# Optimization experiments

Hardware: AMD Instinct MI355X
Metric: run time of the kernel (lower is better)

The kernel has to match this reference:

```python
import jax, jax.numpy as jnp
import numpy as np

EPS = 1e-07


def setup_inputs() -> dict:
    key = jax.random.key(0)
    k1, k2, k3, k4, k5, k6 = jax.random.split(key, 6)
    B, S, E = 128, 512, 64  # batch, seq_len == n_items, emb_size
    user_emb = jax.random.normal(k1, (B, S, E), dtype=jnp.float32)
    item_emb = jax.random.normal(k2, (B, S, E), dtype=jnp.float32)
    cluster_weights = jax.random.uniform(k3, (B, S, 1), dtype=jnp.float32)
    # binary keep-mask over sequence positions (multiplicative)
    last_item_mask = (jax.random.uniform(k4, (B, 1, S)) > 0.5).astype(jnp.float32)
    proj_w = jax.random.normal(k5, (1, 1), dtype=jnp.float32)
    proj_b = jax.random.normal(k6, (1,), dtype=jnp.float32)
    return {
        "user_emb": user_emb,
        "item_emb": item_emb,
        "cluster_weights": cluster_weights,
        "last_item_mask": last_item_mask,
        "proj_w": proj_w,
        "proj_b": proj_b,
    }


def reference(user_emb, item_emb, cluster_weights, last_item_mask, proj_w, proj_b):
    # L2-normalize with clamped norm (matches torch.clamp(norm, 1e-7))
    u = user_emb / jnp.maximum(jnp.linalg.norm(user_emb, axis=-1, keepdims=True), EPS)
    v = item_emb / jnp.maximum(jnp.linalg.norm(item_emb, axis=-1, keepdims=True), EPS)
    # cosine sim: [B, n_items, seq_len] (n_items == seq_len == S)
    cos = jnp.einsum("bse,bne->bns", u, v)
    # cluster_weights [B,S,1] broadcasts over the seq_len axis, indexed by dim1
    # (faithful to torch broadcast of [B,N,S,1] * [B,S,1,1] with N == S)
    sims = cos * cluster_weights  # [B,N,S]
    # Linear(1,1) + sigmoid applied elementwise (scalar affine)
    sims = jax.nn.sigmoid(sims * proj_w[0, 0] + proj_b[0])
    # permute to [B, seq_len, n_items], mask [B,1,S] broadcasts over last axis
    sims = jnp.swapaxes(sims, 1, 2) * last_item_mask
    # max over dim 2 -> [B, seq_len]
    return jnp.max(sims, axis=2)
```

## Files before the change

kernel.cpp:

```cpp
#include <hip/hip_runtime.h>
#include <hip/hip_bf16.h>
#include <math.h>

#define B_ 128
#define S_ 512
#define E_ 64
#define PAD_ 72

typedef short bf16x8 __attribute__((ext_vector_type(8)));
typedef float f32x4 __attribute__((ext_vector_type(4)));

__device__ __forceinline__ unsigned short f2b(float f) {
  __hip_bfloat16 h = __float2bfloat16(f);
  unsigned short u;
  __builtin_memcpy(&u, &h, 2);
  return u;
}

__device__ __forceinline__ void norm16_coalesced(
    const float* __restrict__ src,
    const float* __restrict__ scl,
    float w0, int c, int g, int lane,
    unsigned short* __restrict__ lds_base) {
  f32x4 x[4];
  float sn[4];
#pragma unroll
  for (int i = 0; i < 4; ++i) x[i] = *(const f32x4*)(src + i * 256 + lane * 4);
#pragma unroll
  for (int i = 0; i < 4; ++i)
    sn[i] = scl ? scl[i * 4 + g] * w0 : 1.0f;
#pragma unroll
  for (int i = 0; i < 4; ++i) {
    float ss = x[i][0] * x[i][0] + x[i][1] * x[i][1] +
               x[i][2] * x[i][2] + x[i][3] * x[i][3];
    ss += __shfl_xor(ss, 1); ss += __shfl_xor(ss, 2);
    ss += __shfl_xor(ss, 4); ss += __shfl_xor(ss, 8);
    float s = sn[i] / fmaxf(sqrtf(ss), 1e-7f);
    ushort4 o;
    o.x = f2b(x[i][0] * s); o.y = f2b(x[i][1] * s);
    o.z = f2b(x[i][2] * s); o.w = f2b(x[i][3] * s);
    *(ushort4*)(lds_base + (size_t)(i * 4 + g) * PAD_ + c * 4) = o;
  }
}

__global__ __launch_bounds__(1024) void fused_kernel(
    const float* __restrict__ ue, const float* __restrict__ ve,
    const float* __restrict__ cw, const float* __restrict__ mask,
    const float* __restrict__ pw, const float* __restrict__ pb,
    float* __restrict__ out) {
  __shared__ unsigned short vlds[S_ * PAD_];
  __shared__ unsigned short ulds[256 * PAD_];
  __shared__ float comb[4][256];

  const int bx = blockIdx.x;
  const int b = (bx & 7) * 16 + (bx >> 4);
  const int shalf = (bx >> 3) & 1;

  const int tid = threadIdx.x;
  const int wv = tid >> 6;
  const int lane = tid & 63;
  const int c = lane & 15;
  const int g = lane >> 4;
  const int ws = wv >> 2;
  const int wn = wv & 3;

  const float w0 = pw[0];
  const float* __restrict__ vb = ve + (size_t)b * S_ * E_;
  const float* __restrict__ cwb = cw + (size_t)b * S_;
  const float* __restrict__ ub = ue + ((size_t)b * S_ + shalf * 256) * E_;
  const float* __restrict__ mb = mask + (size_t)b * S_;

  const int vown = shalf * 256 + wv * 16;
  const int voth = (1 - shalf) * 256 + wv * 16;
  const int urow = wv * 16;

  float pen[8];
#pragma unroll
  for (int j = 0; j < 4; ++j) {
    pen[j] = (mb[(shalf * 16 + wn * 4 + j) * 16 + c] > 0.5f) ? 0.0f : -1e30f;
    pen[4 + j] =
        (mb[((1 - shalf) * 16 + wn * 4 + j) * 16 + c] > 0.5f) ? 0.0f : -1e30f;
  }

  norm16_coalesced(vb + (size_t)vown * E_, cwb + vown, w0, c, g, lane,
                   vlds + (size_t)vown * PAD_);
  norm16_coalesced(ub + (size_t)urow * E_, nullptr, 1.0f, c, g, lane,
                   ulds + (size_t)urow * PAD_);

  __syncthreads();

  const float* psrc = vb + (size_t)voth * E_;
  f32x4 y[4];
#pragma unroll
  for (int i = 0; i < 4; ++i) y[i] = *(const f32x4*)(psrc + i * 256 + lane * 4);
  float cwo[4];
#pragma unroll
  for (int i = 0; i < 4; ++i) cwo[i] = cwb[voth + i * 4 + g];

  const unsigned short* urp = ulds + (size_t)(ws * 64 + c) * PAD_ + g * 8;
  bf16x8 a[4][2];
#pragma unroll
  for (int st = 0; st < 4; ++st) {
    a[st][0] = *(const bf16x8*)(urp + st * 16 * PAD_);
    a[st][1] = *(const bf16x8*)(urp + st * 16 * PAD_ + 32);
  }

  float r[4][4];
#pragma unroll
  for (int st = 0; st < 4; ++st)
#pragma unroll
    for (int i = 0; i < 4; ++i) r[st][i] = -INFINITY;

#pragma unroll
  for (int j = 0; j < 4; ++j) {
    const int it = shalf * 16 + wn * 4 + j;
    const unsigned short* vr = vlds + (size_t)(it * 16 + c) * PAD_ + g * 8;
    bf16x8 b0 = *(const bf16x8*)(vr);
    bf16x8 b1 = *(const bf16x8*)(vr + 32);
    f32x4 ci = {pen[j], pen[j], pen[j], pen[j]};
#pragma unroll
    for (int st = 0; st < 4; ++st) {
      f32x4 acc = __builtin_amdgcn_mfma_f32_16x16x32_bf16(a[st][0], b0, ci, 0, 0, 0);
      acc = __builtin_amdgcn_mfma_f32_16x16x32_bf16(a[st][1], b1, acc, 0, 0, 0);
      r[st][0] = fmaxf(r[st][0], acc[0]);
      r[st][1] = fmaxf(r[st][1], acc[1]);
      r[st][2] = fmaxf(r[st][2], acc[2]);
      r[st][3] = fmaxf(r[st][3], acc[3]);
    }
  }

#pragma unroll
  for (int i = 0; i < 4; ++i) {
    float ss = y[i][0] * y[i][0] + y[i][1] * y[i][1] +
               y[i][2] * y[i][2] + y[i][3] * y[i][3];
    ss += __shfl_xor(ss, 1); ss += __shfl_xor(ss, 2);
    ss += __shfl_xor(ss, 4); ss += __shfl_xor(ss, 8);
    float s = (w0 * cwo[i]) / fmaxf(sqrtf(ss), 1e-7f);
    ushort4 o;
    o.x = f2b(y[i][0] * s); o.y = f2b(y[i][1] * s);
    o.z = f2b(y[i][2] * s); o.w = f2b(y[i][3] * s);
    *(ushort4*)(vlds + (size_t)(voth + i * 4 + g) * PAD_ + c * 4) = o;
  }

  __syncthreads();

#pragma unroll
  for (int j = 0; j < 4; ++j) {
    const int it = (1 - shalf) * 16 + wn * 4 + j;
    const unsigned short* vr = vlds + (size_t)(it * 16 + c) * PAD_ + g * 8;
    bf16x8 b0 = *(const bf16x8*)(vr);
    bf16x8 b1 = *(const bf16x8*)(vr + 32);
    f32x4 ci = {pen[4 + j], pen[4 + j], pen[4 + j], pen[4 + j]};
#pragma unroll
    for (int st = 0; st < 4; ++st) {
      f32x4 acc = __builtin_amdgcn_mfma_f32_16x16x32_bf16(a[st][0], b0, ci, 0, 0, 0);
      acc = __builtin_amdgcn_mfma_f32_16x16x32_bf16(a[st][1], b1, acc, 0, 0, 0);
      r[st][0] = fmaxf(r[st][0], acc[0]);
      r[st][1] = fmaxf(r[st][1], acc[1]);
      r[st][2] = fmaxf(r[st][2], acc[2]);
      r[st][3] = fmaxf(r[st][3], acc[3]);
    }
  }

#pragma unroll
  for (int st = 0; st < 4; ++st)
#pragma unroll
    for (int i = 0; i < 4; ++i) {
      float v = r[st][i];
      v = fmaxf(v, __shfl_xor(v, 1)); v = fmaxf(v, __shfl_xor(v, 2));
      v = fmaxf(v, __shfl_xor(v, 4)); v = fmaxf(v, __shfl_xor(v, 8));
      r[st][i] = v;
    }

  if (c == 0) {
#pragma unroll
    for (int st = 0; st < 4; ++st)
#pragma unroll
      for (int i = 0; i < 4; ++i)
        comb[wn][ws * 64 + st * 16 + g * 4 + i] = r[st][i];
  }

  __syncthreads();

  if (tid < 256) {
    float v = fmaxf(fmaxf(comb[0][tid], comb[1][tid]),
                    fmaxf(comb[2][tid], comb[3][tid]));
    float bias = pb[0];
    out[(size_t)b * S_ + shalf * 256 + tid] =
        (v < -1e29f) ? 0.0f : 1.0f / (1.0f + expf(-(v + bias)));
  }
}

extern "C" void kernel_launch(void* const* d_in, const int* in_sizes, int n_in,
                              void* d_out, int out_size, void* d_ws, size_t ws_size,
                              hipStream_t stream) {
  const float* ue = (const float*)d_in[0];
  const float* ve = (const float*)d_in[1];
  const float* cw = (const float*)d_in[2];
  const float* mask = (const float*)d_in[3];
  const float* pw = (const float*)d_in[4];
  const float* pb = (const float*)d_in[5];
  float* out = (float*)d_out;

  hipLaunchKernelGGL(fused_kernel, dim3(2 * B_), dim3(1024), 0, stream,
                     ue, ve, cw, mask, pw, pb, out);
}
```

Baseline: 17.53 us.

## Load user rows straight into MFMA fragments and defer normalization past max

User embeddings are no longer normalized into a shared-memory tile. Each lane loads its raw rows straight into bf16 MFMA A-fragments and computes the row inverse-norm with cross-lane shuffles. Because the per-row scale is positive, it is applied after the max reduction instead of before the matmul. This removes the user LDS buffer, its writes and reads, and cuts LDS footprint. The costs are less coalesced global loads, unnormalized values in bf16, and a looser masked-row sentinel threshold to absorb the scaled penalty.

```diff
diff --git a/kernel.cpp b/kernel.cpp
--- a/kernel.cpp
+++ b/kernel.cpp
@@ -17,25 +17,20 @@
   return u;
 }
 
-__device__ __forceinline__ void norm16_coalesced(
-    const float* __restrict__ src,
-    const float* __restrict__ scl,
-    float w0, int c, int g, int lane,
-    unsigned short* __restrict__ lds_base) {
+__device__ __forceinline__ void norm16_v(const float* __restrict__ src,
+                                         const float* __restrict__ cwp,
+                                         float w0, int c, int g, int lane,
+                                         unsigned short* __restrict__ lds_base) {
   f32x4 x[4];
-  float sn[4];
 #pragma unroll
   for (int i = 0; i < 4; ++i) x[i] = *(const f32x4*)(src + i * 256 + lane * 4);
-#pragma unroll
-  for (int i = 0; i < 4; ++i)
-    sn[i] = scl ? scl[i * 4 + g] * w0 : 1.0f;
 #pragma unroll
   for (int i = 0; i < 4; ++i) {
     float ss = x[i][0] * x[i][0] + x[i][1] * x[i][1] +
                x[i][2] * x[i][2] + x[i][3] * x[i][3];
     ss += __shfl_xor(ss, 1); ss += __shfl_xor(ss, 2);
     ss += __shfl_xor(ss, 4); ss += __shfl_xor(ss, 8);
-    float s = sn[i] / fmaxf(sqrtf(ss), 1e-7f);
+    float s = (w0 * cwp[i * 4 + g]) / fmaxf(sqrtf(ss), 1e-7f);
     ushort4 o;
     o.x = f2b(x[i][0] * s); o.y = f2b(x[i][1] * s);
     o.z = f2b(x[i][2] * s); o.w = f2b(x[i][3] * s);
@@ -49,7 +44,6 @@
     const float* __restrict__ pw, const float* __restrict__ pb,
     float* __restrict__ out) {
   __shared__ unsigned short vlds[S_ * PAD_];
-  __shared__ unsigned short ulds[256 * PAD_];
   __shared__ float comb[4][256];
 
   const int bx = blockIdx.x;
@@ -72,7 +66,30 @@
 
   const int vown = shalf * 256 + wv * 16;
   const int voth = (1 - shalf) * 256 + wv * 16;
-  const int urow = wv * 16;
+
+  bf16x8 a[4][2];
+  float rn[4];
+#pragma unroll
+  for (int st = 0; st < 4; ++st) {
+    const float* r_ = ub + (size_t)(ws * 64 + st * 16 + c) * E_;
+    f32x4 u0 = *(const f32x4*)(r_ + 8 * g);
+    f32x4 u1 = *(const f32x4*)(r_ + 8 * g + 4);
+    f32x4 u2 = *(const f32x4*)(r_ + 32 + 8 * g);
+    f32x4 u3 = *(const f32x4*)(r_ + 32 + 8 * g + 4);
+    float ss = 0.f;
+#pragma unroll
+    for (int j = 0; j < 4; ++j)
+      ss = fmaf(u0[j], u0[j],
+           fmaf(u1[j], u1[j], fmaf(u2[j], u2[j], fmaf(u3[j], u3[j], ss))));
+    ss += __shfl_xor(ss, 16);
+    ss += __shfl_xor(ss, 32);
+    rn[st] = 1.0f / fmaxf(sqrtf(ss), 1e-7f);
+#pragma unroll
+    for (int j = 0; j < 4; ++j) {
+      a[st][0][j] = (short)f2b(u0[j]); a[st][0][4 + j] = (short)f2b(u1[j]);
+      a[st][1][j] = (short)f2b(u2[j]); a[st][1][4 + j] = (short)f2b(u3[j]);
+    }
+  }
 
   float pen[8];
 #pragma unroll
@@ -82,10 +99,8 @@
         (mb[((1 - shalf) * 16 + wn * 4 + j) * 16 + c] > 0.5f) ? 0.0f : -1e30f;
   }
 
-  norm16_coalesced(vb + (size_t)vown * E_, cwb + vown, w0, c, g, lane,
-                   vlds + (size_t)vown * PAD_);
-  norm16_coalesced(ub + (size_t)urow * E_, nullptr, 1.0f, c, g, lane,
-                   ulds + (size_t)urow * PAD_);
+  norm16_v(vb + (size_t)vown * E_, cwb + vown, w0, c, g, lane,
+           vlds + (size_t)vown * PAD_);
 
   __syncthreads();
 
@@ -96,14 +111,6 @@
   float cwo[4];
 #pragma unroll
   for (int i = 0; i < 4; ++i) cwo[i] = cwb[voth + i * 4 + g];
-
-  const unsigned short* urp = ulds + (size_t)(ws * 64 + c) * PAD_ + g * 8;
-  bf16x8 a[4][2];
-#pragma unroll
-  for (int st = 0; st < 4; ++st) {
-    a[st][0] = *(const bf16x8*)(urp + st * 16 * PAD_);
-    a[st][1] = *(const bf16x8*)(urp + st * 16 * PAD_ + 32);
-  }
 
   float r[4][4];
 #pragma unroll
@@ -169,7 +176,8 @@
       float v = r[st][i];
       v = fmaxf(v, __shfl_xor(v, 1)); v = fmaxf(v, __shfl_xor(v, 2));
       v = fmaxf(v, __shfl_xor(v, 4)); v = fmaxf(v, __shfl_xor(v, 8));
-      r[st][i] = v;
+      float un = __shfl(rn[st], g * 4 + i);
+      r[st][i] = v * un;
     }
 
   if (c == 0) {
@@ -187,7 +195,7 @@
                     fmaxf(comb[2][tid], comb[3][tid]));
     float bias = pb[0];
     out[(size_t)b * S_ + shalf * 256 + tid] =
-        (v < -1e29f) ? 0.0f : 1.0f / (1.0f + expf(-(v + bias)));
+        (v < -1e27f) ? 0.0f : 1.0f / (1.0f + expf(-(v + bias)));
   }
 }
 
```

Result: slower. 25.38 us (+44.8%).
